# Optimization experiments

Measured on AMD Instinct MI355X. Metric: run time of the kernel, lower is better.

Reference implementation:

```python
import jax, jax.numpy as jnp
import numpy as np

B, N, G, C = 4, 4000, 64, 91
H, W = 800.0, 1333.0
FG_THRESH, BG_THRESH = 0.5, 0.5
SCORE_THRESH, NMS_THRESH = 0.05, 0.5
DET_PER_IMG = 100
PRE_NMS_TOPK = 2048   # candidates entering NMS per image
MIN_SIZE = 0.01
BBOX_XFORM_CLIP = float(np.log(1000.0 / 16.0))
WX, WY, WW, WH = 10.0, 10.0, 5.0, 5.0  # bbox_reg_weights


def _rand_boxes(key, shape):
    k1, k2 = jax.random.split(key)
    xy = jax.random.uniform(k1, shape[:-1] + (2,)) * jnp.array([W * 0.8, H * 0.8], jnp.float32)
    wh = jax.random.uniform(k2, shape[:-1] + (2,)) * jnp.array([W * 0.2, H * 0.2], jnp.float32) + 2.0
    return jnp.concatenate([xy, xy + wh], axis=-1)


def setup_inputs():
    key = jax.random.key(0)
    ks = jax.random.split(key, 5)
    proposals = _rand_boxes(ks[0], (B, N, 4))
    gt_boxes = _rand_boxes(ks[1], (B, G, 4))
    gt_labels = jax.random.randint(ks[2], (B, G), 1, C)
    class_logits = jax.random.normal(ks[3], (B, N, C), dtype=jnp.float32)
    box_regression = jax.random.normal(ks[4], (B, N, C * 4), dtype=jnp.float32) * 0.1
    return {"proposals": proposals, "gt_boxes": gt_boxes, "gt_labels": gt_labels,
            "class_logits": class_logits, "box_regression": box_regression}


def box_iou(a, b):
    # a [A,4], b [B,4] -> [A,B]
    area_a = (a[:, 2] - a[:, 0]) * (a[:, 3] - a[:, 1])
    area_b = (b[:, 2] - b[:, 0]) * (b[:, 3] - b[:, 1])
    lt = jnp.maximum(a[:, None, :2], b[None, :, :2])
    rb = jnp.minimum(a[:, None, 2:], b[None, :, 2:])
    wh = jnp.clip(rb - lt, 0.0)
    inter = wh[..., 0] * wh[..., 1]
    return inter / (area_a[:, None] + area_b[None, :] - inter)


def encode(gt, prop):
    # BoxCoder.encode with weights (10,10,5,5)
    pw = prop[:, 2] - prop[:, 0]; ph = prop[:, 3] - prop[:, 1]
    px = prop[:, 0] + 0.5 * pw;  py = prop[:, 1] + 0.5 * ph
    gw = gt[:, 2] - gt[:, 0];    gh = gt[:, 3] - gt[:, 1]
    gx = gt[:, 0] + 0.5 * gw;    gy = gt[:, 1] + 0.5 * gh
    return jnp.stack([WX * (gx - px) / pw, WY * (gy - py) / ph,
                      WW * jnp.log(gw / pw), WH * jnp.log(gh / ph)], axis=1)


def decode(deltas, boxes):
    # deltas [N,C,4], boxes [N,4] -> [N,C,4]
    pw = boxes[:, 2] - boxes[:, 0]; ph = boxes[:, 3] - boxes[:, 1]
    px = boxes[:, 0] + 0.5 * pw;    py = boxes[:, 1] + 0.5 * ph
    dx = deltas[..., 0] / WX; dy = deltas[..., 1] / WY
    dw = jnp.minimum(deltas[..., 2] / WW, BBOX_XFORM_CLIP)
    dh = jnp.minimum(deltas[..., 3] / WH, BBOX_XFORM_CLIP)
    cx = dx * pw[:, None] + px[:, None]; cy = dy * ph[:, None] + py[:, None]
    w = jnp.exp(dw) * pw[:, None];       h = jnp.exp(dh) * ph[:, None]
    return jnp.stack([cx - 0.5 * w, cy - 0.5 * h, cx + 0.5 * w, cy + 0.5 * h], axis=-1)


def _image_fwd(prop, gt_b, gt_l, logits, regr):
    # --- assign_targets_to_proposals (with add_gt_proposals) ---
    props_all = jnp.concatenate([prop, gt_b], axis=0)          # [N+G,4]
    iou = box_iou(gt_b, props_all)                             # [G,N+G]
    matched_vals = iou.max(axis=0)
    matches = iou.argmax(axis=0)
    lbl = jnp.where(matched_vals >= FG_THRESH, gt_l[matches],
                    jnp.where(matched_vals < BG_THRESH, 0, -1))
    reg_targets = encode(gt_b[matches], props_all)             # [N+G,4]

    # --- postprocess_detections: decode + softmax + per-class NMS ---
    deltas = regr.reshape(N, C, 4)
    pb = decode(deltas, prop)                                  # [N,C,4]
    pb = jnp.stack([jnp.clip(pb[..., 0], 0.0, W), jnp.clip(pb[..., 1], 0.0, H),
                    jnp.clip(pb[..., 2], 0.0, W), jnp.clip(pb[..., 3], 0.0, H)], axis=-1)
    scores = jax.nn.softmax(logits, axis=-1)                   # [N,C]
    boxes_f = pb[:, 1:].reshape(-1, 4)                         # drop background class
    scores_f = scores[:, 1:].reshape(-1)
    labels_f = jnp.broadcast_to(jnp.arange(1, C), (N, C - 1)).reshape(-1)
    wf = boxes_f[:, 2] - boxes_f[:, 0]; hf = boxes_f[:, 3] - boxes_f[:, 1]
    valid = (scores_f > SCORE_THRESH) & (wf >= MIN_SIZE) & (hf >= MIN_SIZE)
    masked = jnp.where(valid, scores_f, -1.0)
    top_vals, top_idx = jax.lax.top_k(masked, PRE_NMS_TOPK)    # score-sorted candidates
    cb = boxes_f[top_idx]; cl = labels_f[top_idx]; cs = scores_f[top_idx]
    cv = top_vals > 0.0
    # batched_nms via per-class coordinate offset
    off = cl.astype(cb.dtype) * (max(W, H) + 1.0)
    ob = cb + off[:, None]
    iou_c = box_iou(ob, ob)                                    # [M,M]
    order = jnp.arange(PRE_NMS_TOPK)

    def body(i, keep):
        sup = keep[i] & (iou_c[i] > NMS_THRESH) & (order > i)
        return keep & ~sup

    keep = jax.lax.fori_loop(0, PRE_NMS_TOPK, body, cv)
    rank = jnp.cumsum(keep) - 1
    out_pos = jnp.where(keep & (rank < DET_PER_IMG), rank, DET_PER_IMG)  # OOB -> drop
    det_b = jnp.zeros((DET_PER_IMG, 4), cb.dtype).at[out_pos].set(cb, mode='drop')
    det_s = jnp.zeros((DET_PER_IMG,), cs.dtype).at[out_pos].set(cs, mode='drop')
    det_l = jnp.zeros((DET_PER_IMG,), cl.dtype).at[out_pos].set(cl, mode='drop')
    det = jnp.concatenate([det_b, det_s[:, None]], axis=-1)    # [K,5]
    return det, reg_targets, lbl, det_l


def reference(proposals, gt_boxes, gt_labels, class_logits, box_regression):
    return jax.vmap(_image_fwd)(proposals, gt_boxes, gt_labels, class_logits, box_regression)
```

## Files before the change

kernel.cpp:

```cpp
#include <hip/hip_runtime.h>
#include <cstdint>
#include <cstddef>

#define Bn   4
#define Nn   4000
#define Gn   64
#define Cn   91
#define FGC  90
#define RPW  8
#define BLKROWS 32
#define NBLKI 125
#define CAPSEG 160
#define SLOTSI (NBLKI*CAPSEG)
#define SLICE 1250
#define SELCAP 4096
#define MSEL 2048
#define DETK 100

__device__ __constant__ float kW = 1333.0f;
__device__ __constant__ float kH = 800.0f;
#define XCLIP 4.135166556742356f
#define OFFMUL 1334.0f

#define NB 9216
#define SBIAS 0x3D400000u

typedef __attribute__((ext_vector_type(2))) unsigned long long u64x2;

#define OUT_DET  0
#define OUT_REG  (Bn*DETK*5)
#define OUT_LBL  (OUT_REG + Bn*(Nn+Gn)*4)
#define OUT_DETL (OUT_LBL + Bn*(Nn+Gn))

#define ZERO_N16 (147712/16)

__device__ __forceinline__ void decode_box(float4 p, float4 d,
                                           float& bx1, float& by1, float& bx2, float& by2) {
    float pw = p.z - p.x, ph = p.w - p.y;
    float px = p.x + 0.5f * pw, py = p.y + 0.5f * ph;
    float dx = d.x / 10.0f, dy = d.y / 10.0f;
    float dw = fminf(d.z / 5.0f, XCLIP), dh = fminf(d.w / 5.0f, XCLIP);
    float cx = dx * pw + px, cy = dy * ph + py;
    float w = expf(dw) * pw, h = expf(dh) * ph;
    bx1 = fminf(fmaxf(cx - 0.5f * w, 0.0f), kW);
    by1 = fminf(fmaxf(cy - 0.5f * h, 0.0f), kH);
    bx2 = fminf(fmaxf(cx + 0.5f * w, 0.0f), kW);
    by2 = fminf(fmaxf(cy + 0.5f * h, 0.0f), kH);
}

__device__ __forceinline__ unsigned score_bucket(unsigned sb) {
    unsigned h = (sb - SBIAS) >> 12;
    return h > (NB - 1) ? (NB - 1) : h;
}

__global__ __launch_bounds__(256) void zero_k(uint4* __restrict__ p) {
    int i = blockIdx.x * 256 + threadIdx.x;
    if (i < ZERO_N16) p[i] = make_uint4(0, 0, 0, 0);
}

__global__ __launch_bounds__(256) void fused_cand_k(const float* __restrict__ logits,
                                                    const float* __restrict__ regr,
                                                    const float* __restrict__ props,
                                                    unsigned long long* __restrict__ keys,
                                                    unsigned int* __restrict__ cnt,
                                                    unsigned int* __restrict__ hist) {
    __shared__ unsigned lcnt;
    int wave = threadIdx.x >> 6, lane = threadIdx.x & 63;
    int blk = blockIdx.x;
    if (threadIdx.x == 0) lcnt = 0;
    int rowbase = blk * BLKROWS + wave * RPW;
    int b = blk / NBLKI;
    int nbase = rowbase - b * Nn;
    bool has1 = (lane + 64) < Cn;
    const float* z = logits + (size_t)rowbase * Cn;
    float v0[RPW], v1[RPW], m[RPW], e[RPW], t0[RPW], t1[RPW];
    #pragma unroll
    for (int r = 0; r < RPW; ++r) {
        v0[r] = z[r * Cn + lane];
        v1[r] = has1 ? z[r * Cn + lane + 64] : -INFINITY;
        m[r] = fmaxf(v0[r], v1[r]);
    }
    #pragma unroll
    for (int o = 32; o; o >>= 1) {
        #pragma unroll
        for (int r = 0; r < RPW; ++r) m[r] = fmaxf(m[r], __shfl_xor(m[r], o));
    }
    #pragma unroll
    for (int r = 0; r < RPW; ++r) {
        t0[r] = expf(v0[r] - m[r]);
        t1[r] = has1 ? expf(v1[r] - m[r]) : 0.0f;
        e[r] = t0[r] + t1[r];
    }
    #pragma unroll
    for (int o = 32; o; o >>= 1) {
        #pragma unroll
        for (int r = 0; r < RPW; ++r) e[r] += __shfl_xor(e[r], o);
    }
    unsigned long long keyA[RPW], keyB[RPW];
    bool vA[RPW], vB[RPW];
    #pragma unroll
    for (int r = 0; r < RPW; ++r) {
        float s0 = t0[r] / e[r];
        float s1 = has1 ? (t1[r] / e[r]) : 0.0f;
        vA[r] = (lane >= 1) && (s0 > 0.05f);
        vB[r] = has1 && (s1 > 0.05f);
        keyA[r] = 0; keyB[r] = 0;
        float4 p = make_float4(0.f, 0.f, 0.f, 0.f);
        if (vA[r] || vB[r]) p = ((const float4*)props)[rowbase + r];
        if (vA[r]) {
            int c = lane;
            float4 d = ((const float4*)regr)[(size_t)(rowbase + r) * Cn + c];
            float bx1, by1, bx2, by2;
            decode_box(p, d, bx1, by1, bx2, by2);
            vA[r] = (bx2 - bx1 >= 0.01f) && (by2 - by1 >= 0.01f);
            unsigned idx = (unsigned)((nbase + r) * FGC + c - 1);
            keyA[r] = ((unsigned long long)__float_as_uint(s0) << 32) | (unsigned long long)(~idx);
            if (vA[r]) atomicAdd(&hist[b * NB + score_bucket(__float_as_uint(s0))], 1u);
        }
        if (vB[r]) {
            int c = lane + 64;
            float4 d = ((const float4*)regr)[(size_t)(rowbase + r) * Cn + c];
            float bx1, by1, bx2, by2;
            decode_box(p, d, bx1, by1, bx2, by2);
            vB[r] = (bx2 - bx1 >= 0.01f) && (by2 - by1 >= 0.01f);
            unsigned idx = (unsigned)((nbase + r) * FGC + c - 1);
            keyB[r] = ((unsigned long long)__float_as_uint(s1) << 32) | (unsigned long long)(~idx);
            if (vB[r]) atomicAdd(&hist[b * NB + score_bucket(__float_as_uint(s1))], 1u);
        }
    }
    __syncthreads();
    unsigned long long mk[2 * RPW];
    #pragma unroll
    for (int r = 0; r < RPW; ++r) { mk[2*r] = __ballot(vA[r]); mk[2*r+1] = __ballot(vB[r]); }
    unsigned tot = 0, pre[2 * RPW];
    #pragma unroll
    for (int q = 0; q < 2 * RPW; ++q) { pre[q] = tot; tot += (unsigned)__popcll(mk[q]); }
    if (tot) {
        unsigned base = 0;
        if (lane == 0) base = atomicAdd(&lcnt, tot);
        base = __shfl(base, 0);
        unsigned long long lmask = (lane == 63) ? (~0ull >> 1) : ((1ull << lane) - 1);
        size_t segbase = (size_t)blk * CAPSEG;
        #pragma unroll
        for (int r = 0; r < RPW; ++r) {
            if (vA[r]) {
                unsigned pos = base + pre[2*r] + (unsigned)__popcll(mk[2*r] & lmask);
                if (pos < CAPSEG) keys[segbase + pos] = keyA[r];
            }
            if (vB[r]) {
                unsigned pos = base + pre[2*r+1] + (unsigned)__popcll(mk[2*r+1] & lmask);
                if (pos < CAPSEG) keys[segbase + pos] = keyB[r];
            }
        }
    }
    __syncthreads();
    if (threadIdx.x == 0) cnt[blk] = lcnt;
}

__global__ __launch_bounds__(256) void compact_k(const unsigned long long* __restrict__ keys,
                                                 const unsigned int* __restrict__ cnt,
                                                 const unsigned int* __restrict__ hist,
                                                 unsigned long long* __restrict__ sel,
                                                 unsigned int* __restrict__ cnt2) {
    int b = blockIdx.x >> 4, blk = blockIdx.x & 15;
    int tid = threadIdx.x, lane = tid & 63, wv = tid >> 6;
    __shared__ unsigned wtot[4], wt2[4], sscnt[NBLKI];
    __shared__ unsigned sT, sbase;

    const uint4* h4 = (const uint4*)(hist + b * NB);
    unsigned hc[36]; unsigned ssum = 0;
    #pragma unroll
    for (int q = 0; q < 9; ++q) {
        uint4 t4 = h4[tid * 9 + q];
        hc[q*4+0] = t4.x; hc[q*4+1] = t4.y; hc[q*4+2] = t4.z; hc[q*4+3] = t4.w;
        ssum += t4.x + t4.y + t4.z + t4.w;
    }
    unsigned x = ssum;
    #pragma unroll
    for (int o = 1; o < 64; o <<= 1) { unsigned v = __shfl_down(x, o); if (lane + o < 64) x += v; }
    if (lane == 0) wtot[wv] = x;
    if (tid < NBLKI) { unsigned c = cnt[b * NBLKI + tid]; sscnt[tid] = c > CAPSEG ? CAPSEG : c; }
    if (tid == 0) sT = NB;
    __syncthreads();
    unsigned above = 0, total = 0;
    #pragma unroll
    for (int i2 = 0; i2 < 4; ++i2) { unsigned w2 = wtot[i2]; total += w2; if (i2 > wv) above += w2; }
    unsigned K2 = total < MSEL ? total : MSEL;
    if (K2 == 0) return;
    unsigned run = (x - ssum) + above;
    #pragma unroll
    for (int q = 35; q >= 0; --q) {
        unsigned c = hc[q], lo = run;
        run += c;
        if (lo < K2 && K2 <= run) sT = (unsigned)(tid * 36 + q);
    }
    __syncthreads();
    unsigned T = sT;

    unsigned long long kk[5]; bool vv[5]; unsigned c2 = 0;
    #pragma unroll
    for (int it = 0; it < 5; ++it) {
        vv[it] = false; kk[it] = 0;
        int off = it * 256 + tid;
        if (off < SLICE) {
            int g = blk * SLICE + off;
            int seg = g / CAPSEG, s = g - seg * CAPSEG;
            if (s < (int)sscnt[seg]) {
                unsigned long long k = keys[(size_t)b * SLOTSI + g];
                if (score_bucket((unsigned)(k >> 32)) >= T) { kk[it] = k; vv[it] = true; ++c2; }
            }
        }
    }
    unsigned inc = c2;
    #pragma unroll
    for (int o = 1; o < 64; o <<= 1) { unsigned v = __shfl_up(inc, o); if (lane >= o) inc += v; }
    unsigned excl = inc - c2;
    if (lane == 63) wt2[wv] = inc;
    __syncthreads();
    if (tid == 0) {
        unsigned tot = wt2[0] + wt2[1] + wt2[2] + wt2[3];
        sbase = tot ? atomicAdd(&cnt2[b], tot) : 0u;
    }
    __syncthreads();
    unsigned pos = sbase + excl;
    #pragma unroll
    for (int i2 = 0; i2 < 4; ++i2) if (i2 < wv) pos += wt2[i2];
    unsigned long long* selb = sel + (size_t)b * SELCAP;
    #pragma unroll
    for (int it = 0; it < 5; ++it) {
        if (vv[it]) { if (pos < SELCAP) selb[pos] = kk[it]; ++pos; }
    }
}

__global__ __launch_bounds__(256) void rank_sel_k(const unsigned long long* __restrict__ sel,
                                                  const unsigned int* __restrict__ cnt2,
                                                  const float* __restrict__ props,
                                                  const float* __restrict__ regr,
                                                  float* __restrict__ cb, float* __restrict__ ob,
                                                  float* __restrict__ sc, int* __restrict__ lab) {
    int b = blockIdx.x >> 6, blk = blockIdx.x & 63;
    unsigned n2 = cnt2[b]; if (n2 > SELCAP) n2 = SELCAP;
    if ((unsigned)(blk * 64) >= n2) return;
    int lane = threadIdx.x & 63, wv = threadIdx.x >> 6;
    int sub = blk * 64 + lane;
    __shared__ __align__(16) unsigned long long skk[SELCAP + 2];
    __shared__ unsigned pc[4][64];
    unsigned n2p = (n2 + 1) & ~1u;
    const unsigned long long* selb = sel + (size_t)b * SELCAP;
    for (unsigned s2 = threadIdx.x; s2 < n2p; s2 += 256)
        skk[s2] = (s2 < n2) ? selb[s2] : 0ull;
    __syncthreads();
    unsigned long long mk = (sub < (int)n2) ? skk[sub] : ~0ull;
    bool act = (sub < (int)n2) && ((mk >> 32) != 0ull);
    unsigned pairs = n2p >> 1;
    unsigned Q = (pairs + 3) >> 2;
    unsigned jb = wv * Q, je = jb + Q; if (je > pairs) je = pairs;
    const u64x2* sk2 = (const u64x2*)skk;
    unsigned cntg = 0;
    for (unsigned j = jb; j < je; ++j) {
        u64x2 kk = sk2[j];
        cntg += (unsigned)(kk.x > mk) + (unsigned)(kk.y > mk);
    }
    pc[wv][lane] = cntg;
    __syncthreads();
    if (wv == 0) {
        unsigned rank = pc[0][lane] + pc[1][lane] + pc[2][lane] + pc[3][lane];
        if (act && rank < MSEL) {
            int t = b * MSEL + (int)rank;
            unsigned idx = ~(unsigned)mk;
            int n = idx / FGC, cm1 = idx - n * FGC;
            int c = cm1 + 1;
            float score = __uint_as_float((unsigned)(mk >> 32));
            int row = b * Nn + n;
            float4 p = ((const float4*)props)[row];
            float4 d = ((const float4*)regr)[(size_t)row * Cn + c];
            float bx1, by1, bx2, by2;
            decode_box(p, d, bx1, by1, bx2, by2);
            float off = (float)c * OFFMUL;
            cb[t * 4 + 0] = bx1; cb[t * 4 + 1] = by1; cb[t * 4 + 2] = bx2; cb[t * 4 + 3] = by2;
            ob[t * 4 + 0] = bx1 + off; ob[t * 4 + 1] = by1 + off;
            ob[t * 4 + 2] = bx2 + off; ob[t * 4 + 3] = by2 + off;
            sc[t] = score; lab[t] = c;
        }
    }
}

__global__ __launch_bounds__(256) void nmsmat_k(const float* __restrict__ ob,
                                                unsigned long long* __restrict__ M) {
    int blk = blockIdx.x;
    int b = blk >> 8, rc = (blk >> 5) & 7, w = blk & 31;
    int i = rc * 256 + threadIdx.x;
    size_t mi = ((size_t)b * MSEL + i) * 32 + w;
    if (w * 64 + 63 <= rc * 256) {
        M[mi] = 0ull;
        return;
    }
    __shared__ float4 sj[64];
    const float4* obf4 = (const float4*)(ob + (size_t)b * MSEL * 4);
    if (threadIdx.x < 64) sj[threadIdx.x] = obf4[w * 64 + threadIdx.x];
    __syncthreads();
    float4 bi = obf4[i];
    float areai = (bi.z - bi.x) * (bi.w - bi.y);
    unsigned long long bits = 0ull;
    #pragma unroll 16
    for (int tt = 0; tt < 64; ++tt) {
        int j = w * 64 + tt;
        float4 bj = sj[tt];
        float xx1 = fmaxf(bi.x, bj.x), yy1 = fmaxf(bi.y, bj.y);
        float xx2 = fminf(bi.z, bj.z), yy2 = fminf(bi.w, bj.w);
        float iw = fmaxf(xx2 - xx1, 0.0f), ih = fmaxf(yy2 - yy1, 0.0f);
        float inter = iw * ih;
        float areaj = (bj.z - bj.x) * (bj.w - bj.y);
        float iou = inter / (areai + areaj - inter);
        if ((iou > 0.5f) && (j > i)) bits |= (1ull << tt);
    }
    M[mi] = bits;
}

__global__ __launch_bounds__(64) void scan_k(const unsigned long long* __restrict__ M,
                                             const unsigned int* __restrict__ cnt2,
                                             const float* __restrict__ cb,
                                             const float* __restrict__ sc,
                                             const int* __restrict__ lab,
                                             float* __restrict__ out) {
    int b = blockIdx.x, lane = threadIdx.x;
    const bool ld = lane < 32;
    unsigned n2 = cnt2[b]; if (n2 > SELCAP) n2 = SELCAP;
    int validN = (int)(n2 < MSEL ? n2 : MSEL);
    unsigned long long keep = 0ull;
    if (ld) {
        int base = lane * 64;
        keep = (base + 64 <= validN) ? ~0ull
             : (base >= validN ? 0ull : ((1ull << (validN - base)) - 1ull));
    }
    unsigned kLo = (unsigned)keep, kHi = (unsigned)(keep >> 32);
    __shared__ int keptIdx[DETK];
    const unsigned long long* Mb = M + (size_t)b * MSEL * 32;
    int kcount = 0;
    unsigned long long Abuf[16], Bbuf[16];
    #pragma unroll
    for (int k = 0; k < 16; ++k) Abuf[k] = ld ? Mb[(size_t)k * 32 + lane] : 0ull;
    for (int g = 0; g < 128; g += 2) {
        #pragma unroll
        for (int k = 0; k < 16; ++k)
            Bbuf[k] = ld ? Mb[(size_t)((g + 1) * 16 + k) * 32 + lane] : 0ull;
        {
            int base = g * 16;
            int rl = base >> 6, sh = base & 31;
            unsigned half = (base >> 5) & 1;
            #pragma unroll
            for (int k = 0; k < 16; ++k) {
                unsigned kw = half ? kHi : kLo;
                unsigned bitv = (__builtin_amdgcn_readlane(kw, rl) >> (sh + k)) & 1u;
                if (bitv) {
                    unsigned long long m = Abuf[k];
                    kLo &= ~(unsigned)m; kHi &= ~(unsigned)(m >> 32);
                    if (kcount < DETK && lane == 0) keptIdx[kcount] = base + k;
                    ++kcount;
                }
            }
        }
        if (kcount >= DETK) break;
        if (g + 2 < 128) {
            #pragma unroll
            for (int k = 0; k < 16; ++k)
                Abuf[k] = ld ? Mb[(size_t)((g + 2) * 16 + k) * 32 + lane] : 0ull;
        }
        {
            int base = (g + 1) * 16;
            int rl = base >> 6, sh = base & 31;
            unsigned half = (base >> 5) & 1;
            #pragma unroll
            for (int k = 0; k < 16; ++k) {
                unsigned kw = half ? kHi : kLo;
                unsigned bitv = (__builtin_amdgcn_readlane(kw, rl) >> (sh + k)) & 1u;
                if (bitv) {
                    unsigned long long m = Bbuf[k];
                    kLo &= ~(unsigned)m; kHi &= ~(unsigned)(m >> 32);
                    if (kcount < DETK && lane == 0) keptIdx[kcount] = base + k;
                    ++kcount;
                }
            }
        }
        if (kcount >= DETK) break;
    }
    __syncthreads();
    int kept100 = kcount < DETK ? kcount : DETK;
    for (int r = lane; r < kept100; r += 64) {
        int i = keptIdx[r];
        int slot = b * MSEL + i;
        float* dr = out + OUT_DET + ((size_t)b * DETK + r) * 5;
        dr[0] = cb[slot * 4 + 0]; dr[1] = cb[slot * 4 + 1];
        dr[2] = cb[slot * 4 + 2]; dr[3] = cb[slot * 4 + 3];
        dr[4] = sc[slot];
        out[OUT_DETL + b * DETK + r] = (float)lab[slot];
    }
    for (int r = kept100 + lane; r < DETK; r += 64) {
        float* dr = out + OUT_DET + ((size_t)b * DETK + r) * 5;
        dr[0] = dr[1] = dr[2] = dr[3] = dr[4] = 0.0f;
        out[OUT_DETL + b * DETK + r] = 0.0f;
    }
}

__global__ __launch_bounds__(256) void assign_k(const float* __restrict__ props,
                                                const float* __restrict__ gtb,
                                                const int* __restrict__ gtl,
                                                float* __restrict__ out) {
    __shared__ float4 sg[Gn];
    int b = blockIdx.y;
    int p = blockIdx.x * 256 + threadIdx.x;
    if (threadIdx.x < Gn) sg[threadIdx.x] = ((const float4*)(gtb + (size_t)b * Gn * 4))[threadIdx.x];
    __syncthreads();
    if (p >= Nn + Gn) return;
    float4 pb = (p < Nn) ? ((const float4*)(props + (size_t)b * Nn * 4))[p] : sg[p - Nn];
    float areap = (pb.z - pb.x) * (pb.w - pb.y);
    float best = -1.0f; int bi = 0;
    #pragma unroll 4
    for (int g = 0; g < Gn; ++g) {
        float4 gb = sg[g];
        float xx1 = fmaxf(gb.x, pb.x), yy1 = fmaxf(gb.y, pb.y);
        float xx2 = fminf(gb.z, pb.z), yy2 = fminf(gb.w, pb.w);
        float iw = fmaxf(xx2 - xx1, 0.0f), ih = fmaxf(yy2 - yy1, 0.0f);
        float inter = iw * ih;
        float areag = (gb.z - gb.x) * (gb.w - gb.y);
        float iou = inter / (areag + areap - inter);
        if (iou > best) { best = iou; bi = g; }
    }
    float4 gb = sg[bi];
    float pw = pb.z - pb.x, ph = pb.w - pb.y;
    float px = pb.x + 0.5f * pw, py = pb.y + 0.5f * ph;
    float gw = gb.z - gb.x, gh = gb.w - gb.y;
    float gx = gb.x + 0.5f * gw, gy = gb.y + 0.5f * gh;
    float* rr = out + OUT_REG + ((size_t)b * (Nn + Gn) + p) * 4;
    rr[0] = 10.0f * (gx - px) / pw;
    rr[1] = 10.0f * (gy - py) / ph;
    rr[2] = 5.0f * logf(gw / pw);
    rr[3] = 5.0f * logf(gh / ph);
    out[OUT_LBL + (size_t)b * (Nn + Gn) + p] = (best >= 0.5f) ? (float)gtl[b * Gn + bi] : 0.0f;
}

extern "C" void kernel_launch(void* const* d_in, const int* in_sizes, int n_in,
                              void* d_out, int out_size, void* d_ws, size_t ws_size,
                              hipStream_t stream) {
    const float* props  = (const float*)d_in[0];
    const float* gtb    = (const float*)d_in[1];
    const int*   gtl    = (const int*)d_in[2];
    const float* logits = (const float*)d_in[3];
    const float* regr   = (const float*)d_in[4];
    float* out = (float*)d_out;

    char* w = (char*)d_ws;
    unsigned int* cnt2          = (unsigned int*)(w + 0);
    unsigned int* hist          = (unsigned int*)(w + 256);
    unsigned int* cnt           = (unsigned int*)(w + 147712);
    unsigned long long* sel     = (unsigned long long*)(w + 149760);
    unsigned long long* keys    = (unsigned long long*)(w + 280832);
    float* cb                   = (float*)(w + 920832);
    float* ob                   = (float*)(w + 1051904);
    float* sc                   = (float*)(w + 1182976);
    int* lab                    = (int*)(w + 1215744);
    unsigned long long* M       = (unsigned long long*)(w + 1248512);
    (void)ws_size; (void)in_sizes; (void)n_in; (void)out_size;

    zero_k<<<(ZERO_N16 + 255) / 256, 256, 0, stream>>>((uint4*)w);
    fused_cand_k<<<Bn * NBLKI, 256, 0, stream>>>(logits, regr, props, keys, cnt, hist);
    compact_k<<<Bn * 16, 256, 0, stream>>>(keys, cnt, hist, sel, cnt2);
    rank_sel_k<<<Bn * 64, 256, 0, stream>>>(sel, cnt2, props, regr, cb, ob, sc, lab);
    nmsmat_k<<<Bn * 256, 256, 0, stream>>>(ob, M);
    scan_k<<<Bn, 64, 0, stream>>>(M, cnt2, cb, sc, lab, out);
    assign_k<<<dim3((Nn + Gn + 255) / 256, Bn), 256, 0, stream>>>(props, gtb, gtl, out);
}
```

Measured before the change: 87.85 us.

## Defer box decode to compaction and fuse assignment with workspace zeroing

The GT assignment kernel is merged with the workspace-zeroing kernel into one launch, which removes a separate kernel launch at the tail. Box decoding and the min-size filter move out of the candidate scoring pass into compaction, so regression deltas are gathered only for keys above the histogram threshold. Blocks now cover 16 rows instead of 32, with matching segment capacity and slice sizes. The histogram now counts candidates before the min-size filter, so the selection threshold can differ slightly from the reference when tiny boxes occur.

Result: faster. 80.68 us (-8.2%).

```diff
diff --git a/kernel.cpp b/kernel.cpp
--- a/kernel.cpp
+++ b/kernel.cpp
@@ -7,12 +7,12 @@
 #define Gn   64
 #define Cn   91
 #define FGC  90
-#define RPW  8
-#define BLKROWS 32
-#define NBLKI 125
-#define CAPSEG 160
+#define RPW  4
+#define BLKROWS 16
+#define NBLKI 250
+#define CAPSEG 128
 #define SLOTSI (NBLKI*CAPSEG)
-#define SLICE 1250
+#define SLICE 2000
 #define SELCAP 4096
 #define MSEL 2048
 #define DETK 100
@@ -33,6 +33,7 @@
 #define OUT_DETL (OUT_LBL + Bn*(Nn+Gn))
 
 #define ZERO_N16 (147712/16)
+#define ZERO_BLKS 37
 
 __device__ __forceinline__ void decode_box(float4 p, float4 d,
                                            float& bx1, float& by1, float& bx2, float& by2) {
@@ -53,14 +54,51 @@
     return h > (NB - 1) ? (NB - 1) : h;
 }
 
-__global__ __launch_bounds__(256) void zero_k(uint4* __restrict__ p) {
-    int i = blockIdx.x * 256 + threadIdx.x;
-    if (i < ZERO_N16) p[i] = make_uint4(0, 0, 0, 0);
+__global__ __launch_bounds__(256) void pre_k(const float* __restrict__ props,
+                                             const float* __restrict__ gtb,
+                                             const int* __restrict__ gtl,
+                                             float* __restrict__ out,
+                                             uint4* __restrict__ zp) {
+    int blk = blockIdx.x;
+    if (blk >= 64) {
+        int i = (blk - 64) * 256 + threadIdx.x;
+        if (i < ZERO_N16) zp[i] = make_uint4(0, 0, 0, 0);
+        return;
+    }
+    __shared__ float4 sg[Gn];
+    int b = blk >> 4;
+    int p = (blk & 15) * 256 + threadIdx.x;
+    if (threadIdx.x < Gn) sg[threadIdx.x] = ((const float4*)(gtb + (size_t)b * Gn * 4))[threadIdx.x];
+    __syncthreads();
+    if (p >= Nn + Gn) return;
+    float4 pb = (p < Nn) ? ((const float4*)(props + (size_t)b * Nn * 4))[p] : sg[p - Nn];
+    float areap = (pb.z - pb.x) * (pb.w - pb.y);
+    float best = -1.0f; int bi = 0;
+    #pragma unroll 4
+    for (int g = 0; g < Gn; ++g) {
+        float4 gb = sg[g];
+        float xx1 = fmaxf(gb.x, pb.x), yy1 = fmaxf(gb.y, pb.y);
+        float xx2 = fminf(gb.z, pb.z), yy2 = fminf(gb.w, pb.w);
+        float iw = fmaxf(xx2 - xx1, 0.0f), ih = fmaxf(yy2 - yy1, 0.0f);
+        float inter = iw * ih;
+        float areag = (gb.z - gb.x) * (gb.w - gb.y);
+        float iou = inter / (areag + areap - inter);
+        if (iou > best) { best = iou; bi = g; }
+    }
+    float4 gb = sg[bi];
+    float pw = pb.z - pb.x, ph = pb.w - pb.y;
+    float px = pb.x + 0.5f * pw, py = pb.y + 0.5f * ph;
+    float gw = gb.z - gb.x, gh = gb.w - gb.y;
+    float gx = gb.x + 0.5f * gw, gy = gb.y + 0.5f * gh;
+    float* rr = out + OUT_REG + ((size_t)b * (Nn + Gn) + p) * 4;
+    rr[0] = 10.0f * (gx - px) / pw;
+    rr[1] = 10.0f * (gy - py) / ph;
+    rr[2] = 5.0f * logf(gw / pw);
+    rr[3] = 5.0f * logf(gh / ph);
+    out[OUT_LBL + (size_t)b * (Nn + Gn) + p] = (best >= 0.5f) ? (float)gtl[b * Gn + bi] : 0.0f;
 }
 
 __global__ __launch_bounds__(256) void fused_cand_k(const float* __restrict__ logits,
-                                                    const float* __restrict__ regr,
-                                                    const float* __restrict__ props,
                                                     unsigned long long* __restrict__ keys,
                                                     unsigned int* __restrict__ cnt,
                                                     unsigned int* __restrict__ hist) {
@@ -104,29 +142,12 @@
         float s1 = has1 ? (t1[r] / e[r]) : 0.0f;
         vA[r] = (lane >= 1) && (s0 > 0.05f);
         vB[r] = has1 && (s1 > 0.05f);
-        keyA[r] = 0; keyB[r] = 0;
-        float4 p = make_float4(0.f, 0.f, 0.f, 0.f);
-        if (vA[r] || vB[r]) p = ((const float4*)props)[rowbase + r];
-        if (vA[r]) {
-            int c = lane;
-            float4 d = ((const float4*)regr)[(size_t)(rowbase + r) * Cn + c];
-            float bx1, by1, bx2, by2;
-            decode_box(p, d, bx1, by1, bx2, by2);
-            vA[r] = (bx2 - bx1 >= 0.01f) && (by2 - by1 >= 0.01f);
-            unsigned idx = (unsigned)((nbase + r) * FGC + c - 1);
-            keyA[r] = ((unsigned long long)__float_as_uint(s0) << 32) | (unsigned long long)(~idx);
-            if (vA[r]) atomicAdd(&hist[b * NB + score_bucket(__float_as_uint(s0))], 1u);
-        }
-        if (vB[r]) {
-            int c = lane + 64;
-            float4 d = ((const float4*)regr)[(size_t)(rowbase + r) * Cn + c];
-            float bx1, by1, bx2, by2;
-            decode_box(p, d, bx1, by1, bx2, by2);
-            vB[r] = (bx2 - bx1 >= 0.01f) && (by2 - by1 >= 0.01f);
-            unsigned idx = (unsigned)((nbase + r) * FGC + c - 1);
-            keyB[r] = ((unsigned long long)__float_as_uint(s1) << 32) | (unsigned long long)(~idx);
-            if (vB[r]) atomicAdd(&hist[b * NB + score_bucket(__float_as_uint(s1))], 1u);
-        }
+        unsigned idxA = (unsigned)((nbase + r) * FGC + lane - 1);
+        unsigned idxB = (unsigned)((nbase + r) * FGC + lane + 63);
+        keyA[r] = ((unsigned long long)__float_as_uint(s0) << 32) | (unsigned long long)(~idxA);
+        keyB[r] = ((unsigned long long)__float_as_uint(s1) << 32) | (unsigned long long)(~idxB);
+        if (vA[r]) atomicAdd(&hist[b * NB + score_bucket(__float_as_uint(s0))], 1u);
+        if (vB[r]) atomicAdd(&hist[b * NB + score_bucket(__float_as_uint(s1))], 1u);
     }
     __syncthreads();
     unsigned long long mk[2 * RPW];
@@ -160,6 +181,8 @@
 __global__ __launch_bounds__(256) void compact_k(const unsigned long long* __restrict__ keys,
                                                  const unsigned int* __restrict__ cnt,
                                                  const unsigned int* __restrict__ hist,
+                                                 const float* __restrict__ props,
+                                                 const float* __restrict__ regr,
                                                  unsigned long long* __restrict__ sel,
                                                  unsigned int* __restrict__ cnt2) {
     int b = blockIdx.x >> 4, blk = blockIdx.x & 15;
@@ -197,17 +220,28 @@
     __syncthreads();
     unsigned T = sT;
 
-    unsigned long long kk[5]; bool vv[5]; unsigned c2 = 0;
-    #pragma unroll
-    for (int it = 0; it < 5; ++it) {
+    unsigned long long kk[8]; bool vv[8]; unsigned c2 = 0;
+    #pragma unroll
+    for (int it = 0; it < 8; ++it) {
         vv[it] = false; kk[it] = 0;
         int off = it * 256 + tid;
         if (off < SLICE) {
             int g = blk * SLICE + off;
-            int seg = g / CAPSEG, s = g - seg * CAPSEG;
+            int seg = g >> 7, s = g & (CAPSEG - 1);
             if (s < (int)sscnt[seg]) {
                 unsigned long long k = keys[(size_t)b * SLOTSI + g];
-                if (score_bucket((unsigned)(k >> 32)) >= T) { kk[it] = k; vv[it] = true; ++c2; }
+                if (score_bucket((unsigned)(k >> 32)) >= T) {
+                    unsigned idx = ~(unsigned)k;
+                    int n = idx / FGC, cm1 = idx - n * FGC;
+                    int row = b * Nn + n;
+                    float4 p = ((const float4*)props)[row];
+                    float4 d = ((const float4*)regr)[(size_t)row * Cn + cm1 + 1];
+                    float bx1, by1, bx2, by2;
+                    decode_box(p, d, bx1, by1, bx2, by2);
+                    if ((bx2 - bx1 >= 0.01f) && (by2 - by1 >= 0.01f)) {
+                        kk[it] = k; vv[it] = true; ++c2;
+                    }
+                }
             }
         }
     }
@@ -227,7 +261,7 @@
     for (int i2 = 0; i2 < 4; ++i2) if (i2 < wv) pos += wt2[i2];
     unsigned long long* selb = sel + (size_t)b * SELCAP;
     #pragma unroll
-    for (int it = 0; it < 5; ++it) {
+    for (int it = 0; it < 8; ++it) {
         if (vv[it]) { if (pos < SELCAP) selb[pos] = kk[it]; ++pos; }
     }
 }
@@ -402,43 +436,6 @@
     }
 }
 
-__global__ __launch_bounds__(256) void assign_k(const float* __restrict__ props,
-                                                const float* __restrict__ gtb,
-                                                const int* __restrict__ gtl,
-                                                float* __restrict__ out) {
-    __shared__ float4 sg[Gn];
-    int b = blockIdx.y;
-    int p = blockIdx.x * 256 + threadIdx.x;
-    if (threadIdx.x < Gn) sg[threadIdx.x] = ((const float4*)(gtb + (size_t)b * Gn * 4))[threadIdx.x];
-    __syncthreads();
-    if (p >= Nn + Gn) return;
-    float4 pb = (p < Nn) ? ((const float4*)(props + (size_t)b * Nn * 4))[p] : sg[p - Nn];
-    float areap = (pb.z - pb.x) * (pb.w - pb.y);
-    float best = -1.0f; int bi = 0;
-    #pragma unroll 4
-    for (int g = 0; g < Gn; ++g) {
-        float4 gb = sg[g];
-        float xx1 = fmaxf(gb.x, pb.x), yy1 = fmaxf(gb.y, pb.y);
-        float xx2 = fminf(gb.z, pb.z), yy2 = fminf(gb.w, pb.w);
-        float iw = fmaxf(xx2 - xx1, 0.0f), ih = fmaxf(yy2 - yy1, 0.0f);
-        float inter = iw * ih;
-        float areag = (gb.z - gb.x) * (gb.w - gb.y);
-        float iou = inter / (areag + areap - inter);
-        if (iou > best) { best = iou; bi = g; }
-    }
-    float4 gb = sg[bi];
-    float pw = pb.z - pb.x, ph = pb.w - pb.y;
-    float px = pb.x + 0.5f * pw, py = pb.y + 0.5f * ph;
-    float gw = gb.z - gb.x, gh = gb.w - gb.y;
-    float gx = gb.x + 0.5f * gw, gy = gb.y + 0.5f * gh;
-    float* rr = out + OUT_REG + ((size_t)b * (Nn + Gn) + p) * 4;
-    rr[0] = 10.0f * (gx - px) / pw;
-    rr[1] = 10.0f * (gy - py) / ph;
-    rr[2] = 5.0f * logf(gw / pw);
-    rr[3] = 5.0f * logf(gh / ph);
-    out[OUT_LBL + (size_t)b * (Nn + Gn) + p] = (best >= 0.5f) ? (float)gtl[b * Gn + bi] : 0.0f;
-}
-
 extern "C" void kernel_launch(void* const* d_in, const int* in_sizes, int n_in,
                               void* d_out, int out_size, void* d_ws, size_t ws_size,
                               hipStream_t stream) {
@@ -453,20 +450,19 @@
     unsigned int* cnt2          = (unsigned int*)(w + 0);
     unsigned int* hist          = (unsigned int*)(w + 256);
     unsigned int* cnt           = (unsigned int*)(w + 147712);
-    unsigned long long* sel     = (unsigned long long*)(w + 149760);
-    unsigned long long* keys    = (unsigned long long*)(w + 280832);
-    float* cb                   = (float*)(w + 920832);
-    float* ob                   = (float*)(w + 1051904);
-    float* sc                   = (float*)(w + 1182976);
-    int* lab                    = (int*)(w + 1215744);
-    unsigned long long* M       = (unsigned long long*)(w + 1248512);
+    unsigned long long* sel     = (unsigned long long*)(w + 151808);
+    unsigned long long* keys    = (unsigned long long*)(w + 282880);
+    float* cb                   = (float*)(w + 1306880);
+    float* ob                   = (float*)(w + 1437952);
+    float* sc                   = (float*)(w + 1569024);
+    int* lab                    = (int*)(w + 1601792);
+    unsigned long long* M       = (unsigned long long*)(w + 1634560);
     (void)ws_size; (void)in_sizes; (void)n_in; (void)out_size;
 
-    zero_k<<<(ZERO_N16 + 255) / 256, 256, 0, stream>>>((uint4*)w);
-    fused_cand_k<<<Bn * NBLKI, 256, 0, stream>>>(logits, regr, props, keys, cnt, hist);
-    compact_k<<<Bn * 16, 256, 0, stream>>>(keys, cnt, hist, sel, cnt2);
+    pre_k<<<64 + ZERO_BLKS, 256, 0, stream>>>(props, gtb, gtl, out, (uint4*)w);
+    fused_cand_k<<<Bn * NBLKI, 256, 0, stream>>>(logits, keys, cnt, hist);
+    compact_k<<<Bn * 16, 256, 0, stream>>>(keys, cnt, hist, props, regr, sel, cnt2);
     rank_sel_k<<<Bn * 64, 256, 0, stream>>>(sel, cnt2, props, regr, cb, ob, sc, lab);
     nmsmat_k<<<Bn * 256, 256, 0, stream>>>(ob, M);
     scan_k<<<Bn, 64, 0, stream>>>(M, cnt2, cb, sc, lab, out);
-    assign_k<<<dim3((Nn + Gn + 255) / 256, Bn), 256, 0, stream>>>(props, gtb, gtl, out);
-}
+}
```
